# Performance work log

Hardware: AMD Instinct MI355X
Metric: run time of the kernel (lower is better)

## Reference

```python
import jax, jax.numpy as jnp
import numpy as np

B, N, NP, NS = 8, 4096, 1024, 32
CF = 64            # input point-feature channels; in_channel = 3 + CF = 67
MLP = [64, 128, 256]
EPS = 1e-5         # BatchNorm eps (torch default)


def setup_inputs() -> dict:
    key = jax.random.key(0)
    ks = jax.random.split(key, 8)
    inp = {
        "xyz": jax.random.normal(ks[0], (B, N, 3), jnp.float32),
        "points": jax.random.normal(ks[1], (B, CF, N), jnp.float32),
        "sample_idx": jax.random.randint(ks[2], (B, NP), 0, N, dtype=jnp.int32),
        "neighbor_idx": jax.random.randint(ks[3], (B, NP, NS), 0, N, dtype=jnp.int32),
    }
    c = 3 + CF
    for i, o in enumerate(MLP):
        wk = jax.random.fold_in(ks[4], i)
        inp[f"W{i}"] = jax.random.normal(wk, (o, c), jnp.float32) * (1.0 / np.sqrt(c))
        inp[f"b{i}"] = jnp.zeros((o,), jnp.float32)
        inp[f"gamma{i}"] = jnp.ones((o,), jnp.float32)
        inp[f"beta{i}"] = jnp.zeros((o,), jnp.float32)
        c = o
    return inp


def _forward(xyz, points, sample_idx, neighbor_idx, params):
    # xyz: (B,N,3)  points: (B,CF,N)
    new_xyz = jnp.take_along_axis(xyz, sample_idx[:, :, None], axis=1)        # (B,NP,3)
    nbr_xyz = jax.vmap(lambda x, idx: x[idx])(xyz, neighbor_idx)               # (B,NP,NS,3)
    rel = nbr_xyz - new_xyz[:, :, None, :]                                     # (B,NP,NS,3)
    nbr_feat = jax.vmap(lambda f, idx: f[:, idx])(points, neighbor_idx)        # (B,CF,NP,NS)
    x = jnp.concatenate([rel.transpose(0, 3, 1, 2), nbr_feat], axis=1)         # (B,3+CF,NP,NS)
    # 1x1 Conv2d -> BatchNorm2d (training-mode batch stats) -> ReLU stack
    for W, b, g, be in params:
        x = jnp.einsum('oc,bcps->bops', W, x) + b[None, :, None, None]
        mu = x.mean(axis=(0, 2, 3), keepdims=True)
        var = x.var(axis=(0, 2, 3), keepdims=True)
        x = g[None, :, None, None] * (x - mu) * jax.lax.rsqrt(var + EPS) + be[None, :, None, None]
        x = jax.nn.relu(x)
    new_points = x.max(axis=-1)                                                # (B,C_out,NP)
    return new_xyz, new_points


def reference(xyz, points, sample_idx, neighbor_idx,
              W0, b0, gamma0, beta0,
              W1, b1, gamma1, beta1,
              W2, b2, gamma2, beta2):
    params = [(W0, b0, gamma0, beta0), (W1, b1, gamma1, beta1), (W2, b2, gamma2, beta2)]
    return _forward(xyz, points, sample_idx, neighbor_idx, params)
```

## Files before the change

kernel.cpp:

```cpp
#include <hip/hip_runtime.h>

typedef unsigned short u16;
typedef unsigned int u32;
typedef __attribute__((ext_vector_type(8))) short short8;
typedef __attribute__((ext_vector_type(16))) float f32x16;

#define BB 8
#define NN 4096
#define NPP 1024
#define NSS 32
#define CFF 64
#define C0 67
#define H0 64
#define H1 128
#define H2 256
#define MTOT (BB*NPP*NSS)
#define BN_EPS 1e-5f
#define INV_M (1.0f/262144.0f)

#define MFMA32(a,b,c) __builtin_amdgcn_mfma_f32_32x32x16_bf16(a,b,c,0,0,0)

__device__ __forceinline__ float bf2f(u16 h){ return __uint_as_float(((u32)h)<<16); }
__device__ __forceinline__ u16 f2bf(float f){
  u32 u = __float_as_uint(f);
  u32 r = (u + 0x7fffu + ((u>>16)&1u)) >> 16;
  return (u16)r;
}
__device__ __forceinline__ u32 pack2(float a, float b){
  return (u32)f2bf(a) | ((u32)f2bf(b)<<16);
}

#define WS_NEED 46280704u

__global__ __launch_bounds__(256) void k_setup(
    const float* __restrict__ xyz, const float* __restrict__ points,
    const int* __restrict__ sidx,
    const float* __restrict__ W0, const float* __restrict__ W1, const float* __restrict__ W2,
    u16* __restrict__ ptsT, u16* __restrict__ Wt0c, u16* __restrict__ Wt1c,
    u16* __restrict__ Wt2c, float* __restrict__ out_newxyz)
{
  int blk = blockIdx.x, tid = threadIdx.x;
  if (blk < 512) {
    __shared__ float t[64][65];
    int b = blk >> 6, n0 = (blk & 63) << 6;
    int nloc = tid & 63, cpart = tid >> 6;
    for (int i = 0; i < 16; ++i) {
      int c = i*4 + cpart;
      t[c][nloc] = points[(size_t)(b*CFF + c)*NN + n0 + nloc];
    }
    __syncthreads();
    int cloc = tid & 63, npart = tid >> 6;
    for (int i = 0; i < 16; ++i) {
      int n = i*4 + npart;
      ptsT[((size_t)(b*NN + n0 + n))*CFF + cloc] = f2bf(t[cloc][n]);
    }
  } else if (blk < 544) {
    int t0 = (blk - 512)*256 + tid;
    int b = t0 >> 10;
    int s = sidx[t0];
    for (int k = 0; k < 3; ++k)
      out_newxyz[(size_t)t0*3 + k] = xyz[((size_t)(b*NN + s))*3 + k];
  } else if (blk == 544) {
    for (int i = 0; i < 24; ++i) {
      int e = i*256 + tid;
      int kc = e >> 9, o = (e >> 3) & 63, j = e & 7, k = kc*8 + j;
      float v = (k < 64) ? W0[o*C0 + 3 + k] : ((k < 67) ? W0[o*C0 + (k - 64)] : 0.f);
      Wt0c[e] = f2bf(v);
    }
  } else if (blk == 545) {
    for (int i = 0; i < 32; ++i) {
      int e = i*256 + tid;
      int kc = e >> 10, n = (e >> 3) & 127, j = e & 7;
      Wt1c[e] = f2bf(W1[n*H0 + kc*8 + j]);
    }
  } else {
    int base = (blk - 546) * 4096;
    for (int i = 0; i < 16; ++i) {
      int e = base + i*256 + tid;
      int kc = e >> 11, n = (e >> 3) & 255, j = e & 7;
      Wt2c[e] = f2bf(W2[n*H1 + kc*8 + j]);
    }
  }
}

__global__ __launch_bounds__(256) void k_xyz_only(
    const float* __restrict__ xyz, const int* __restrict__ sidx, float* __restrict__ out_newxyz)
{
  int t0 = blockIdx.x*256 + threadIdx.x;
  int b = t0 >> 10;
  int s = sidx[t0];
  for (int k = 0; k < 3; ++k)
    out_newxyz[(size_t)t0*3 + k] = xyz[((size_t)(b*NN + s))*3 + k];
}

__global__ __launch_bounds__(256) void k_l0(
    const float* __restrict__ xyz, const int* __restrict__ sidx, const int* __restrict__ nidx,
    const u16* __restrict__ ptsT, const u16* __restrict__ Wt0c,
    u16* __restrict__ y0, float* __restrict__ stats)
{
  __shared__ u16 XLc[12*128*8];
  __shared__ u16 W0c[12*64*8];
  int tid = threadIdx.x;
  int m0 = blockIdx.x * 128;
  int b = m0 >> 15;

  for (int i = 0; i < 3; ++i)
    ((uint4*)W0c)[i*256 + tid] = ((const uint4*)Wt0c)[i*256 + tid];

  int pos = tid & 127, half = tid >> 7;
  int m = m0 + pos;
  int nb = nidx[m];
  {
    const uint4* prow = (const uint4*)(ptsT + ((size_t)(b*NN + nb))*CFF + half*32);
    uint4 h0 = prow[0], h1 = prow[1], h2 = prow[2], h3 = prow[3];
    *(uint4*)&XLc[((half*4+0)*128 + pos)*8] = h0;
    *(uint4*)&XLc[((half*4+1)*128 + pos)*8] = h1;
    *(uint4*)&XLc[((half*4+2)*128 + pos)*8] = h2;
    *(uint4*)&XLc[((half*4+3)*128 + pos)*8] = h3;
    if (half == 0) {
      int p = (m & 32767) >> 5;
      int sp = sidx[b*NPP + p];
      float r0 = xyz[((size_t)(b*NN+nb))*3+0] - xyz[((size_t)(b*NN+sp))*3+0];
      float r1 = xyz[((size_t)(b*NN+nb))*3+1] - xyz[((size_t)(b*NN+sp))*3+1];
      float r2 = xyz[((size_t)(b*NN+nb))*3+2] - xyz[((size_t)(b*NN+sp))*3+2];
      uint4 v = { pack2(r0, r1), pack2(r2, 0.f), 0u, 0u };
      *(uint4*)&XLc[(8*128 + pos)*8] = v;
    } else {
      uint4 z = {0u,0u,0u,0u};
      *(uint4*)&XLc[(9*128 + pos)*8]  = z;
      *(uint4*)&XLc[(10*128 + pos)*8] = z;
      *(uint4*)&XLc[(11*128 + pos)*8] = z;
    }
  }
  __syncthreads();

  int lane = tid & 63, wv = tid >> 6;
  int l31 = lane & 31, kh = lane >> 5;
  int nt = wv & 1, mtb = (wv >> 1) * 2;
  f32x16 acc[2];
  for (int mi = 0; mi < 2; ++mi) for (int r = 0; r < 16; ++r) acc[mi][r] = 0.f;

  for (int kt = 0; kt < 6; ++kt) {
    int ck = kt*2 + kh;
    short8 bfrag = *(const short8*)&W0c[(ck*64 + nt*32 + l31)*8];
    for (int mi = 0; mi < 2; ++mi) {
      short8 afrag = *(const short8*)&XLc[(ck*128 + (mtb+mi)*32 + l31)*8];
      acc[mi] = MFMA32(afrag, bfrag, acc[mi]);
    }
  }

  float s = 0.f, q = 0.f;
  for (int mi = 0; mi < 2; ++mi)
    for (int r = 0; r < 16; ++r) { float y = acc[mi][r]; s += y; q += y*y; }
  s += __shfl_xor(s, 32); q += __shfl_xor(q, 32);
  if (lane < 32) {
    int slot = blockIdx.x & 7;
    atomicAdd(&stats[slot*256 + nt*32 + lane], s);
    atomicAdd(&stats[2048 + slot*256 + nt*32 + lane], q);
  }
  for (int mi = 0; mi < 2; ++mi)
    for (int r = 0; r < 16; ++r) {
      int mm = (mtb+mi)*32 + (r&3) + 8*(r>>2) + 4*kh;
      y0[(size_t)(m0+mm)*H0 + nt*32 + l31] = f2bf(acc[mi][r]);
    }
}

__global__ __launch_bounds__(256) void k_l1s(
    const u16* __restrict__ y0, const u16* __restrict__ Wt1c,
    const float* __restrict__ g0, const float* __restrict__ e0,
    const float* __restrict__ stIn, float* __restrict__ stOut)
{
  __shared__ u16 X0c[8*128*8];
  __shared__ u16 W1c[8*128*8];
  __shared__ float scl0[64], sft0[64];
  int tid = threadIdx.x;
  int m0 = blockIdx.x * 128;

  if (tid < 64) {
    float s = 0.f, q = 0.f;
    for (int sl = 0; sl < 8; ++sl) { s += stIn[sl*256 + tid]; q += stIn[2048 + sl*256 + tid]; }
    float mu = s*INV_M, var = q*INV_M - mu*mu;
    float sc = g0[tid] * rsqrtf(var + BN_EPS);
    scl0[tid] = sc; sft0[tid] = e0[tid] - mu*sc;
  }
  for (int i = 0; i < 4; ++i)
    ((uint4*)W1c)[i*256 + tid] = ((const uint4*)Wt1c)[i*256 + tid];

  int pos = tid & 127, half = tid >> 7;
  {
    const u16* row = y0 + (size_t)(m0 + pos)*H0 + half*32;
    u16 hs[32];
    for (int t = 0; t < 4; ++t) *(uint4*)&hs[t*8] = ((const uint4*)row)[t];
    __syncthreads();
    u16 ob[32];
    for (int j = 0; j < 32; ++j) {
      int c = half*32 + j;
      ob[j] = f2bf(fmaxf(fmaf(scl0[c], bf2f(hs[j]), sft0[c]), 0.f));
    }
    for (int t = 0; t < 4; ++t)
      *(uint4*)&X0c[((half*4+t)*128 + pos)*8] = *(uint4*)&ob[t*8];
  }
  __syncthreads();

  int lane = tid & 63, wv = tid >> 6;
  int l31 = lane & 31, kh = lane >> 5;
  f32x16 acc[4];
  for (int mt = 0; mt < 4; ++mt) for (int r = 0; r < 16; ++r) acc[mt][r] = 0.f;

  for (int kt = 0; kt < 4; ++kt) {
    int ck = kt*2 + kh;
    short8 bfrag = *(const short8*)&W1c[(ck*128 + wv*32 + l31)*8];
    for (int mt = 0; mt < 4; ++mt) {
      short8 afrag = *(const short8*)&X0c[(ck*128 + mt*32 + l31)*8];
      acc[mt] = MFMA32(afrag, bfrag, acc[mt]);
    }
  }

  float s = 0.f, q = 0.f;
  for (int mt = 0; mt < 4; ++mt)
    for (int r = 0; r < 16; ++r) { float y = acc[mt][r]; s += y; q += y*y; }
  s += __shfl_xor(s, 32); q += __shfl_xor(q, 32);
  if (lane < 32) {
    int slot = blockIdx.x & 7;
    atomicAdd(&stOut[slot*256 + wv*32 + lane], s);
    atomicAdd(&stOut[2048 + slot*256 + wv*32 + lane], q);
  }
}

__global__ __launch_bounds__(512) void k_l2f(
    const u16* __restrict__ y0, const u16* __restrict__ Wt1c, const u16* __restrict__ Wt2c,
    const float* __restrict__ g0, const float* __restrict__ e0,
    const float* __restrict__ g1, const float* __restrict__ e1,
    const float* __restrict__ st0, const float* __restrict__ st1, float* __restrict__ stOut,
    u16* __restrict__ mxp, u16* __restrict__ mnp)
{
  __shared__ u16 X0c[8*128*8];
  __shared__ u16 X1c[16*128*8];
  __shared__ float scl0[64], sft0[64], scl1[128], sft1[128];
  int tid = threadIdx.x;
  int m0 = blockIdx.x * 128;

  int lane = tid & 63, w = tid >> 6;
  int l31 = lane & 31, kh = lane >> 5;

  int pos = tid & 127, qh = tid >> 7;
  u16 hs[16];
  {
    const u16* row = y0 + (size_t)(m0 + pos)*H0 + qh*16;
    *(uint4*)&hs[0] = ((const uint4*)row)[0];
    *(uint4*)&hs[8] = ((const uint4*)row)[1];
  }
  int nt1 = w & 3, mh = w >> 2;
  short8 b1[4];
#pragma unroll
  for (int kt = 0; kt < 4; ++kt)
    b1[kt] = *(const short8*)&Wt1c[((kt*2 + kh)*128 + nt1*32 + l31)*8];

  if (tid < 64) {
    float s = 0.f, q = 0.f;
    for (int sl = 0; sl < 8; ++sl) { s += st0[sl*256 + tid]; q += st0[2048 + sl*256 + tid]; }
    float mu = s*INV_M, var = q*INV_M - mu*mu;
    float sc = g0[tid] * rsqrtf(var + BN_EPS);
    scl0[tid] = sc; sft0[tid] = e0[tid] - mu*sc;
  }
  if (tid < 128) {
    float s = 0.f, q = 0.f;
    for (int sl = 0; sl < 8; ++sl) { s += st1[sl*256 + tid]; q += st1[2048 + sl*256 + tid]; }
    float mu = s*INV_M, var = q*INV_M - mu*mu;
    float sc = g1[tid] * rsqrtf(var + BN_EPS);
    scl1[tid] = sc; sft1[tid] = e1[tid] - mu*sc;
  }
  __syncthreads();

  {
    u16 ob[16];
#pragma unroll
    for (int j = 0; j < 16; ++j) {
      int c = qh*16 + j;
      ob[j] = f2bf(fmaxf(fmaf(scl0[c], bf2f(hs[j]), sft0[c]), 0.f));
    }
    *(uint4*)&X0c[((qh*2)*128 + pos)*8]   = *(uint4*)&ob[0];
    *(uint4*)&X0c[((qh*2+1)*128 + pos)*8] = *(uint4*)&ob[8];
  }
  __syncthreads();

  f32x16 acc1[2];
#pragma unroll
  for (int mi = 0; mi < 2; ++mi) for (int r = 0; r < 16; ++r) acc1[mi][r] = 0.f;
#pragma unroll
  for (int kt = 0; kt < 4; ++kt) {
    int ck = kt*2 + kh;
#pragma unroll
    for (int mi = 0; mi < 2; ++mi) {
      short8 afrag = *(const short8*)&X0c[(ck*128 + (mh*2+mi)*32 + l31)*8];
      acc1[mi] = MFMA32(afrag, b1[kt], acc1[mi]);
    }
  }

  short8 b2[8];
#pragma unroll
  for (int k4 = 0; k4 < 8; ++k4)
    b2[k4] = *(const short8*)&Wt2c[((k4*2 + kh)*256 + w*32 + l31)*8];

  {
    int ch1 = nt1*32 + l31;
    int cb = ch1 >> 3, cr = ch1 & 7, sw = cb & 3;
    float sc1 = scl1[ch1], sf1 = sft1[ch1];
#pragma unroll
    for (int mi = 0; mi < 2; ++mi)
#pragma unroll
      for (int r = 0; r < 16; ++r) {
        int mm = (mh*2+mi)*32 + (r&3) + 8*(r>>2) + 4*kh;
        X1c[(cb*128 + (mm ^ sw))*8 + cr] = f2bf(fmaxf(fmaf(sc1, acc1[mi][r], sf1), 0.f));
      }
  }
  __syncthreads();

  f32x16 acc2[4];
#pragma unroll
  for (int mt = 0; mt < 4; ++mt) for (int r = 0; r < 16; ++r) acc2[mt][r] = 0.f;
#pragma unroll
  for (int k4 = 0; k4 < 8; ++k4) {
    int ck = k4*2 + kh;
    int sw = ck & 3;
#pragma unroll
    for (int mt = 0; mt < 4; ++mt) {
      short8 afrag = *(const short8*)&X1c[(ck*128 + ((mt*32 + l31) ^ sw))*8];
      acc2[mt] = MFMA32(afrag, b2[k4], acc2[mt]);
    }
  }

  int ch = w*32 + l31;
  float s = 0.f, q = 0.f;
  float mx[4] = {-3.0e38f,-3.0e38f,-3.0e38f,-3.0e38f};
  float mn[4] = { 3.0e38f, 3.0e38f, 3.0e38f, 3.0e38f};
#pragma unroll
  for (int mt = 0; mt < 4; ++mt)
#pragma unroll
    for (int r = 0; r < 16; ++r) {
      float y = acc2[mt][r];
      s += y; q += y*y;
      mx[mt] = fmaxf(mx[mt], y); mn[mt] = fminf(mn[mt], y);
    }
  s += __shfl_xor(s, 32); q += __shfl_xor(q, 32);
#pragma unroll
  for (int mt = 0; mt < 4; ++mt) {
    mx[mt] = fmaxf(mx[mt], __shfl_xor(mx[mt], 32));
    mn[mt] = fminf(mn[mt], __shfl_xor(mn[mt], 32));
  }
  if (lane < 32) {
    int slot = blockIdx.x & 7;
    atomicAdd(&stOut[slot*256 + ch], s);
    atomicAdd(&stOut[2048 + slot*256 + ch], q);
#pragma unroll
    for (int mt = 0; mt < 4; ++mt) {
      size_t pr = (size_t)blockIdx.x*4 + mt;
      mxp[pr*H2 + ch] = f2bf(mx[mt]);
      mnp[pr*H2 + ch] = f2bf(mn[mt]);
    }
  }
}

__global__ __launch_bounds__(256) void k_final(
    const u16* __restrict__ mxp, const u16* __restrict__ mnp,
    const float* __restrict__ gma, const float* __restrict__ bta,
    const float* __restrict__ stIn, float* __restrict__ out_np)
{
  __shared__ float tmp[256][33];
  int tid = threadIdx.x;
  int b = blockIdx.x >> 5;
  int p0 = (blockIdx.x & 31) * 32;

  float s = 0.f, q = 0.f;
  for (int sl = 0; sl < 8; ++sl) { s += stIn[sl*256 + tid]; q += stIn[2048 + sl*256 + tid]; }
  float mu = s*INV_M, var = q*INV_M - mu*mu;
  float sc = gma[tid] * rsqrtf(var + BN_EPS);
  float sh = bta[tid] - mu*sc;

  for (int pp = 0; pp < 32; ++pp) {
    size_t base = ((size_t)(b*NPP + p0 + pp))*H2 + tid;
    float xv = bf2f(mxp[base]), nv = bf2f(mnp[base]);
    float v = (sc >= 0.f) ? fmaf(sc, xv, sh) : fmaf(sc, nv, sh);
    tmp[tid][pp] = fmaxf(v, 0.f);
  }
  __syncthreads();

  int pl = tid & 31, cg = tid >> 5;
  for (int cc = 0; cc < 32; ++cc) {
    int c = cc*8 + cg;
    out_np[((size_t)b*H2 + c)*NPP + p0 + pl] = tmp[c][pl];
  }
}

extern "C" void kernel_launch(void* const* d_in, const int* in_sizes, int n_in,
                              void* d_out, int out_size, void* d_ws, size_t ws_size,
                              hipStream_t stream)
{
  const float* xyz    = (const float*)d_in[0];
  const float* points = (const float*)d_in[1];
  const int*   sidx   = (const int*)d_in[2];
  const int*   nidx   = (const int*)d_in[3];
  const float* W0 = (const float*)d_in[4];
  const float* g0 = (const float*)d_in[6];
  const float* e0 = (const float*)d_in[7];
  const float* W1 = (const float*)d_in[8];
  const float* g1 = (const float*)d_in[10];
  const float* e1 = (const float*)d_in[11];
  const float* W2 = (const float*)d_in[12];
  const float* g2 = (const float*)d_in[14];
  const float* e2 = (const float*)d_in[15];

  float* out_xyz = (float*)d_out;
  float* out_np  = out_xyz + (size_t)BB*NPP*3;

  if (ws_size < (size_t)WS_NEED) {
    hipMemsetAsync(out_np, 0, (size_t)BB*H2*NPP*4, stream);
    k_xyz_only<<<32, 256, 0, stream>>>(xyz, sidx, out_xyz);
    return;
  }

  char* ws = (char*)d_ws;
  float* stats = (float*)(ws + 0);
  u16*   Wt0c  = (u16*)(ws + 49152);
  u16*   Wt1c  = (u16*)(ws + 61440);
  u16*   Wt2c  = (u16*)(ws + 77824);
  u16*   ptsT  = (u16*)(ws + 143360);
  u16*   y0    = (u16*)(ws + 4337664);
  u16*   mxp   = (u16*)(ws + 37892096);
  u16*   mnp   = (u16*)(ws + 42086400);

  hipMemsetAsync(stats, 0, 3*4096*sizeof(float), stream);
  k_setup<<<554, 256, 0, stream>>>(xyz, points, sidx, W0, W1, W2,
                                   ptsT, Wt0c, Wt1c, Wt2c, out_xyz);
  k_l0<<<MTOT/128, 256, 0, stream>>>(xyz, sidx, nidx, ptsT, Wt0c, y0, stats);
  k_l1s<<<MTOT/128, 256, 0, stream>>>(y0, Wt1c, g0, e0, stats, stats + 4096);
  k_l2f<<<MTOT/128, 512, 0, stream>>>(y0, Wt1c, Wt2c, g0, e0, g1, e1,
                                      stats, stats + 4096, stats + 8192, mxp, mnp);
  k_final<<<256, 256, 0, stream>>>(mxp, mnp, g2, e2, stats + 8192, out_np);
}
```

Before: 172.6 us.

## Compute layer-1 BN statistics via Gram matrix of layer-0 activations

Replaces the layer-1 stats pass, which ran the full 64->128 MFMA GEMM just to collect per-channel sums, with a kernel that accumulates the 64x64 Gram matrix X^T X and the column sums of the normalized layer-0 activations. A small follow-up kernel derives the layer-1 channel sums and sums of squares as W t and the diagonal of W G W^T. This halves the MFMA work of the stats pass and removes per-element stats reduction, at the cost of an extra launch, extra memset, atomics into the Gram buffers, and different floating-point accumulation order. Since b1 is not added here, the result relies on the bias being handled elsewhere, as it was before.

```diff
diff --git a/kernel.cpp b/kernel.cpp
--- a/kernel.cpp
+++ b/kernel.cpp
@@ -30,7 +30,7 @@
   return (u32)f2bf(a) | ((u32)f2bf(b)<<16);
 }
 
-#define WS_NEED 46280704u
+#define WS_NEED 46413824u
 
 __global__ __launch_bounds__(256) void k_setup(
     const float* __restrict__ xyz, const float* __restrict__ points,
@@ -165,65 +165,130 @@
     }
 }
 
-__global__ __launch_bounds__(256) void k_l1s(
-    const u16* __restrict__ y0, const u16* __restrict__ Wt1c,
-    const float* __restrict__ g0, const float* __restrict__ e0,
-    const float* __restrict__ stIn, float* __restrict__ stOut)
-{
-  __shared__ u16 X0c[8*128*8];
-  __shared__ u16 W1c[8*128*8];
+__global__ __launch_bounds__(256) void k_gram(
+    const u16* __restrict__ y0, const float* __restrict__ g0, const float* __restrict__ e0,
+    const float* __restrict__ st0, float* __restrict__ G8, float* __restrict__ t8)
+{
+  __shared__ u16 XT[16*64*8];
   __shared__ float scl0[64], sft0[64];
+  __shared__ float twr[4][32];
   int tid = threadIdx.x;
-  int m0 = blockIdx.x * 128;
 
   if (tid < 64) {
     float s = 0.f, q = 0.f;
-    for (int sl = 0; sl < 8; ++sl) { s += stIn[sl*256 + tid]; q += stIn[2048 + sl*256 + tid]; }
+    for (int sl = 0; sl < 8; ++sl) { s += st0[sl*256 + tid]; q += st0[2048 + sl*256 + tid]; }
     float mu = s*INV_M, var = q*INV_M - mu*mu;
     float sc = g0[tid] * rsqrtf(var + BN_EPS);
     scl0[tid] = sc; sft0[tid] = e0[tid] - mu*sc;
   }
-  for (int i = 0; i < 4; ++i)
-    ((uint4*)W1c)[i*256 + tid] = ((const uint4*)Wt1c)[i*256 + tid];
+  __syncthreads();
 
   int pos = tid & 127, half = tid >> 7;
-  {
-    const u16* row = y0 + (size_t)(m0 + pos)*H0 + half*32;
+  int lane = tid & 63, wv = tid >> 6;
+  int l31 = lane & 31, kh = lane >> 5;
+  int mt = wv >> 1, nt = wv & 1;
+  int rc_w = pos >> 3, jw = pos & 7;
+
+  float tp[32];
+#pragma unroll
+  for (int j = 0; j < 32; ++j) tp[j] = 0.f;
+  f32x16 acc;
+#pragma unroll
+  for (int r = 0; r < 16; ++r) acc[r] = 0.f;
+
+  size_t m0 = (size_t)blockIdx.x * 512;
+  for (int it = 0; it < 4; ++it) {
+    const u16* row = y0 + (m0 + it*128 + pos)*H0 + half*32;
     u16 hs[32];
+#pragma unroll
     for (int t = 0; t < 4; ++t) *(uint4*)&hs[t*8] = ((const uint4*)row)[t];
     __syncthreads();
-    u16 ob[32];
+#pragma unroll
     for (int j = 0; j < 32; ++j) {
       int c = half*32 + j;
-      ob[j] = f2bf(fmaxf(fmaf(scl0[c], bf2f(hs[j]), sft0[c]), 0.f));
-    }
-    for (int t = 0; t < 4; ++t)
-      *(uint4*)&X0c[((half*4+t)*128 + pos)*8] = *(uint4*)&ob[t*8];
-  }
-  __syncthreads();
-
-  int lane = tid & 63, wv = tid >> 6;
-  int l31 = lane & 31, kh = lane >> 5;
-  f32x16 acc[4];
-  for (int mt = 0; mt < 4; ++mt) for (int r = 0; r < 16; ++r) acc[mt][r] = 0.f;
-
-  for (int kt = 0; kt < 4; ++kt) {
-    int ck = kt*2 + kh;
-    short8 bfrag = *(const short8*)&W1c[(ck*128 + wv*32 + l31)*8];
-    for (int mt = 0; mt < 4; ++mt) {
-      short8 afrag = *(const short8*)&X0c[(ck*128 + mt*32 + l31)*8];
-      acc[mt] = MFMA32(afrag, bfrag, acc[mt]);
-    }
-  }
-
-  float s = 0.f, q = 0.f;
-  for (int mt = 0; mt < 4; ++mt)
-    for (int r = 0; r < 16; ++r) { float y = acc[mt][r]; s += y; q += y*y; }
-  s += __shfl_xor(s, 32); q += __shfl_xor(q, 32);
-  if (lane < 32) {
-    int slot = blockIdx.x & 7;
-    atomicAdd(&stOut[slot*256 + wv*32 + lane], s);
-    atomicAdd(&stOut[2048 + slot*256 + wv*32 + lane], q);
+      u16 bv = f2bf(fmaxf(fmaf(scl0[c], bf2f(hs[j]), sft0[c]), 0.f));
+      tp[j] += bf2f(bv);
+      XT[(rc_w*64 + (c ^ (rc_w & 7)))*8 + jw] = bv;
+    }
+    __syncthreads();
+#pragma unroll
+    for (int ks = 0; ks < 8; ++ks) {
+      int rc = ks*2 + kh;
+      short8 af  = *(const short8*)&XT[(rc*64 + ((mt*32 + l31) ^ (rc & 7)))*8];
+      short8 bf_ = *(const short8*)&XT[(rc*64 + ((nt*32 + l31) ^ (rc & 7)))*8];
+      acc = MFMA32(af, bf_, acc);
+    }
+  }
+
+  int slot = blockIdx.x & 7;
+  float* Gq = G8 + slot*4096 + (mt*32)*64 + nt*32;
+#pragma unroll
+  for (int r = 0; r < 16; ++r) {
+    int crow = (r&3) + 8*(r>>2) + 4*kh;
+    atomicAdd(&Gq[crow*64 + l31], acc[r]);
+  }
+#pragma unroll
+  for (int st = 1; st < 64; st <<= 1)
+#pragma unroll
+    for (int j = 0; j < 32; ++j) tp[j] += __shfl_xor(tp[j], st);
+  if (lane == 0) {
+#pragma unroll
+    for (int j = 0; j < 32; ++j) twr[wv][j] = tp[j];
+  }
+  __syncthreads();
+  if (tid < 64) {
+    int h = tid >> 5, j = tid & 31;
+    atomicAdd(&t8[slot*64 + tid], twr[h*2][j] + twr[h*2+1][j]);
+  }
+}
+
+__global__ __launch_bounds__(128) void k_s1f(
+    const float* __restrict__ G8, const float* __restrict__ t8,
+    const u16* __restrict__ Wt1c, float* __restrict__ stOut)
+{
+  __shared__ float Gs[64][64];
+  __shared__ float tl[64];
+  __shared__ float redS[8][16], redQ[8][16];
+  int tid = threadIdx.x;
+#pragma unroll
+  for (int i = 0; i < 32; ++i) {
+    int e = i*128 + tid;
+    float v = 0.f;
+    for (int s = 0; s < 8; ++s) v += G8[s*4096 + e];
+    ((float*)Gs)[e] = v;
+  }
+  if (tid < 64) {
+    float v = 0.f;
+    for (int s = 0; s < 8; ++s) v += t8[s*64 + tid];
+    tl[tid] = v;
+  }
+  __syncthreads();
+
+  int n = blockIdx.x*16 + (tid & 15), g = tid >> 4;
+  float w[64];
+#pragma unroll
+  for (int kc = 0; kc < 8; ++kc)
+#pragma unroll
+    for (int j = 0; j < 8; ++j)
+      w[kc*8 + j] = bf2f(Wt1c[(kc*128 + n)*8 + j]);
+
+  float ps = 0.f, pq = 0.f;
+#pragma unroll
+  for (int ci = 0; ci < 8; ++ci) {
+    int c1 = g*8 + ci;
+    float inner = 0.f;
+#pragma unroll
+    for (int c2 = 0; c2 < 64; ++c2) inner += Gs[c1][c2] * w[c2];
+    pq += w[c1] * inner;
+    ps += w[c1] * tl[c1];
+  }
+  redS[g][tid & 15] = ps; redQ[g][tid & 15] = pq;
+  __syncthreads();
+  if (tid < 16) {
+    float s = 0.f, q = 0.f;
+    for (int g2 = 0; g2 < 8; ++g2) { s += redS[g2][tid]; q += redQ[g2][tid]; }
+    int nn = blockIdx.x*16 + tid;
+    stOut[nn] = s; stOut[2048 + nn] = q;
   }
 }
 
@@ -428,12 +493,16 @@
   u16*   y0    = (u16*)(ws + 4337664);
   u16*   mxp   = (u16*)(ws + 37892096);
   u16*   mnp   = (u16*)(ws + 42086400);
+  float* G8    = (float*)(ws + 46280704);
+  float* t8    = (float*)(ws + 46411776);
 
   hipMemsetAsync(stats, 0, 3*4096*sizeof(float), stream);
+  hipMemsetAsync(ws + 46280704, 0, 133120, stream);
   k_setup<<<554, 256, 0, stream>>>(xyz, points, sidx, W0, W1, W2,
                                    ptsT, Wt0c, Wt1c, Wt2c, out_xyz);
   k_l0<<<MTOT/128, 256, 0, stream>>>(xyz, sidx, nidx, ptsT, Wt0c, y0, stats);
-  k_l1s<<<MTOT/128, 256, 0, stream>>>(y0, Wt1c, g0, e0, stats, stats + 4096);
+  k_gram<<<512, 256, 0, stream>>>(y0, g0, e0, stats, G8, t8);
+  k_s1f<<<8, 128, 0, stream>>>(G8, t8, Wt1c, stats + 4096);
   k_l2f<<<MTOT/128, 512, 0, stream>>>(y0, Wt1c, Wt2c, g0, e0, g1, e1,
                                       stats, stats + 4096, stats + 8192, mxp, mnp);
   k_final<<<256, 256, 0, stream>>>(mxp, mnp, g2, e2, stats + 8192, out_np);
```

Measured after the change: 182.9 us. 1.06x slower.
